# Kernel tuning notes

Hardware: AMD Instinct MI355X
Metric: run time of the kernel (lower is better)

The kernel has to match this reference:

```python
import jax, jax.numpy as jnp
import numpy as np
from jax import lax

T = 1.0      # terminal time
SIGMA = 1.0  # diffusion coefficient
N, D, P, M, H = 16384, 16, 8, 50, 128


def setup_inputs() -> dict:
    key = jax.random.key(0)
    ks = jax.random.split(key, 8)
    scale1 = 1.0 / np.sqrt(1 + D + P)
    scale2 = 1.0 / np.sqrt(H)
    return {
        "initial_states": jax.random.normal(ks[0], (N, D), jnp.float32),
        "initial_values": jax.random.normal(ks[1], (N,), jnp.float32),
        "observations": jax.random.normal(ks[2], (N, P), jnp.float32),
        "noise": jax.random.normal(ks[3], (M, N, D), jnp.float32),
        "W1": jax.random.normal(ks[4], (1 + D + P, H), jnp.float32) * scale1,
        "b1": jnp.zeros((H,), jnp.float32),
        "W2": jax.random.normal(ks[5], (H, H), jnp.float32) * scale2,
        "b2": jnp.zeros((H,), jnp.float32),
        "W3": jax.random.normal(ks[6], (H, D), jnp.float32) * scale2,
        "b3": jnp.zeros((D,), jnp.float32),
    }


def reference(initial_states, initial_values, observations, noise,
              W1, b1, W2, b2, W3, b3):
    """Euler-Maruyama rollout of simulate_SDEs: joint (X, V) SDE with
    per-step Z-network drift. drift b(X) = -X (OU process)."""
    m_steps = noise.shape[0]
    dt = jnp.asarray(T / m_steps, initial_states.dtype)
    sqrt_dt = jnp.sqrt(dt)
    times = jnp.arange(m_steps, dtype=initial_states.dtype) * dt  # time[m]

    def z_net(t, X, Y):
        tcol = jnp.full((X.shape[0], 1), t, X.dtype)
        h = jnp.concatenate([tcol, X, Y], axis=1)      # (N, 1+d+p)
        h = jax.nn.relu(h @ W1 + b1)
        h = jax.nn.relu(h @ W2 + b2)
        return h @ W3 + b3                             # (N, d)

    def step(carry, inp):
        X, V = carry
        eps, t = inp
        Wn = sqrt_dt * eps                             # Brownian increment
        Z = z_net(t, X, observations)
        drift_V = 0.5 * jnp.sum(Z * Z, axis=1)
        V = V + dt * drift_V + jnp.sum(Z * Wn, axis=1)
        X = X + dt * (-X) + SIGMA * Wn                 # b(X) = -X
        return (X, V), None

    (X, V), _ = lax.scan(step, (initial_states, initial_values), (noise, times))
    return X, V
```

## Files before the change

### kernel.cpp

```cpp
#include <hip/hip_runtime.h>

typedef __bf16   bf16x8 __attribute__((ext_vector_type(8)));
typedef float    f32x4  __attribute__((ext_vector_type(4)));
typedef float    f32x2  __attribute__((ext_vector_type(2)));
typedef uint32_t u32x4  __attribute__((ext_vector_type(4)));

constexpr int N_ = 16384;
constexpr int D_ = 16;
constexpr int P_ = 8;
constexpr int H_ = 128;
constexpr int M_ = 50;

__device__ __forceinline__ uint32_t pk_bf16(float a, float b) {
    uint32_t ua = __builtin_bit_cast(uint32_t, a) + 0x8000u;
    uint32_t ub = __builtin_bit_cast(uint32_t, b) + 0x8000u;
    return __builtin_amdgcn_perm(ub, ua, 0x07060302u);
}
__device__ __forceinline__ uint32_t cvtpk(float a, float b) {
    uint32_t r;
    asm("v_cvt_pk_bf16_f32 %0, %1, %2" : "=v"(r) : "v"(a), "v"(b));
    return r;
}
__device__ __forceinline__ uint32_t cvtpk_relu(float a, float b) {
    return cvtpk(fmaxf(a, 0.0f), fmaxf(b, 0.0f));
}

__global__ __launch_bounds__(64, 1)
void sde_fused(const float* __restrict__ X0,
               const float* __restrict__ V0,
               const float* __restrict__ Yobs,
               const float* __restrict__ noise,
               const float* __restrict__ W1, const float* __restrict__ b1,
               const float* __restrict__ W2, const float* __restrict__ b2,
               const float* __restrict__ W3, const float* __restrict__ b3,
               float* __restrict__ out)
{
    const int lane = threadIdx.x;
    const int n    = lane & 15;
    const int q    = lane >> 4;
    const int gr   = blockIdx.x * 16 + n;

    const float dt   = 0.02f;
    const float sqdt = 0.1414213562373095f;

    bf16x8 w1f[8];
#pragma unroll
    for (int ct = 0; ct < 8; ++ct) {
        u32x4 u;
        u[0] = pk_bf16(W1[(1 + q * 4 + 0) * H_ + ct * 16 + n],
                       W1[(1 + q * 4 + 1) * H_ + ct * 16 + n]);
        u[1] = pk_bf16(W1[(1 + q * 4 + 2) * H_ + ct * 16 + n],
                       W1[(1 + q * 4 + 3) * H_ + ct * 16 + n]);
        u[2] = pk_bf16(W1[(17 + q * 2 + 0) * H_ + ct * 16 + n],
                       W1[(17 + q * 2 + 1) * H_ + ct * 16 + n]);
        u[3] = (q == 0) ? pk_bf16(b1[ct * 16 + n], W1[ct * 16 + n]) : 0u;
        w1f[ct] = __builtin_bit_cast(bf16x8, u);
    }
    bf16x8 w2f[8][4];
#pragma unroll
    for (int ct = 0; ct < 8; ++ct)
#pragma unroll
        for (int kt = 0; kt < 4; ++kt) {
            u32x4 u;
#pragma unroll
            for (int w = 0; w < 4; ++w) {
                int h0 = (kt * 2 + (w >> 1)) * 16 + q * 4 + (w & 1) * 2;
                u[w] = pk_bf16(W2[h0 * H_ + ct * 16 + n],
                               W2[(h0 + 1) * H_ + ct * 16 + n]);
            }
            w2f[ct][kt] = __builtin_bit_cast(bf16x8, u);
        }
    bf16x8 w3f[4];
#pragma unroll
    for (int kt = 0; kt < 4; ++kt) {
        u32x4 u;
#pragma unroll
        for (int w = 0; w < 4; ++w) {
            int h0 = (kt * 2 + (w >> 1)) * 16 + q * 4 + (w & 1) * 2;
            u[w] = pk_bf16(W3[h0 * D_ + n], W3[(h0 + 1) * D_ + n]);
        }
        w3f[kt] = __builtin_bit_cast(bf16x8, u);
    }
    f32x4 b2r[8];
#pragma unroll
    for (int ct = 0; ct < 8; ++ct)
#pragma unroll
        for (int r = 0; r < 4; ++r) b2r[ct][r] = b2[ct * 16 + q * 4 + r];
    f32x4 b3r;
#pragma unroll
    for (int r = 0; r < 4; ++r) b3r[r] = b3[q * 4 + r];

    f32x4 x = *(const f32x4*)&X0[gr * D_ + q * 4];
    f32x2 y2 = *(const f32x2*)&Yobs[gr * P_ + q * 2];
    const uint32_t yw = pk_bf16(y2[0], y2[1]);

    const float* npb = noise + (size_t)gr * D_ + q * 4;
    f32x4 e0 = *(const f32x4*)npb;
    f32x4 e1 = *(const f32x4*)(npb + (size_t)N_ * D_);
    float vaccA = 0.0f, vaccB = 0.0f;

#pragma unroll 1
    for (int mm = 0; mm < M_; mm += 2) {
        const int p0 = (mm + 2 < M_) ? (mm + 2) : (M_ - 1);
        const int p1 = (mm + 3 < M_) ? (mm + 3) : (M_ - 1);
        f32x4 eN0 = *(const f32x4*)(npb + (size_t)p0 * N_ * D_);
        f32x4 eN1 = *(const f32x4*)(npb + (size_t)p1 * N_ * D_);

        const float tA = (float)mm * dt;
        const float tB = (float)(mm + 1) * dt;

        f32x4 xB;
#pragma unroll
        for (int r = 0; r < 4; ++r) xB[r] = fmaf(x[r], 0.98f, sqdt * e0[r]);

        u32x4 auA;
        auA[0] = cvtpk(x[0], x[1]);
        auA[1] = cvtpk(x[2], x[3]);
        auA[2] = yw;
        auA[3] = (q == 0) ? cvtpk(1.0f, tA) : 0u;
        bf16x8 a0A = __builtin_bit_cast(bf16x8, auA);
        u32x4 auB;
        auB[0] = cvtpk(xB[0], xB[1]);
        auB[1] = cvtpk(xB[2], xB[3]);
        auB[2] = yw;
        auB[3] = (q == 0) ? cvtpk(1.0f, tB) : 0u;
        bf16x8 a0B = __builtin_bit_cast(bf16x8, auB);

        f32x4 h1cA[8], h1cB[8];
#pragma unroll
        for (int ct = 0; ct < 8; ++ct)
            h1cA[ct] = __builtin_amdgcn_mfma_f32_16x16x32_bf16(
                w1f[ct], a0A, (f32x4){0.f, 0.f, 0.f, 0.f}, 0, 0, 0);
#pragma unroll
        for (int ct = 0; ct < 8; ++ct)
            h1cB[ct] = __builtin_amdgcn_mfma_f32_16x16x32_bf16(
                w1f[ct], a0B, (f32x4){0.f, 0.f, 0.f, 0.f}, 0, 0, 0);

        bf16x8 h1bA[4], h1bB[4];
#pragma unroll
        for (int kt = 0; kt < 4; ++kt) {
            u32x4 u;
            u[0] = cvtpk_relu(h1cA[2 * kt][0], h1cA[2 * kt][1]);
            u[1] = cvtpk_relu(h1cA[2 * kt][2], h1cA[2 * kt][3]);
            u[2] = cvtpk_relu(h1cA[2 * kt + 1][0], h1cA[2 * kt + 1][1]);
            u[3] = cvtpk_relu(h1cA[2 * kt + 1][2], h1cA[2 * kt + 1][3]);
            h1bA[kt] = __builtin_bit_cast(bf16x8, u);
        }
#pragma unroll
        for (int kt = 0; kt < 4; ++kt) {
            u32x4 u;
            u[0] = cvtpk_relu(h1cB[2 * kt][0], h1cB[2 * kt][1]);
            u[1] = cvtpk_relu(h1cB[2 * kt][2], h1cB[2 * kt][3]);
            u[2] = cvtpk_relu(h1cB[2 * kt + 1][0], h1cB[2 * kt + 1][1]);
            u[3] = cvtpk_relu(h1cB[2 * kt + 1][2], h1cB[2 * kt + 1][3]);
            h1bB[kt] = __builtin_bit_cast(bf16x8, u);
        }

        f32x4 h2cA[8], h2cB[8];
#pragma unroll
        for (int ct = 0; ct < 8; ++ct) {
            f32x4 c = b2r[ct];
#pragma unroll
            for (int kt = 0; kt < 4; ++kt)
                c = __builtin_amdgcn_mfma_f32_16x16x32_bf16(
                    w2f[ct][kt], h1bA[kt], c, 0, 0, 0);
            h2cA[ct] = c;
        }
#pragma unroll
        for (int ct = 0; ct < 8; ++ct) {
            f32x4 c = b2r[ct];
#pragma unroll
            for (int kt = 0; kt < 4; ++kt)
                c = __builtin_amdgcn_mfma_f32_16x16x32_bf16(
                    w2f[ct][kt], h1bB[kt], c, 0, 0, 0);
            h2cB[ct] = c;
        }

        bf16x8 h2bA[4], h2bB[4];
#pragma unroll
        for (int kt = 0; kt < 4; ++kt) {
            u32x4 u;
            u[0] = cvtpk_relu(h2cA[2 * kt][0], h2cA[2 * kt][1]);
            u[1] = cvtpk_relu(h2cA[2 * kt][2], h2cA[2 * kt][3]);
            u[2] = cvtpk_relu(h2cA[2 * kt + 1][0], h2cA[2 * kt + 1][1]);
            u[3] = cvtpk_relu(h2cA[2 * kt + 1][2], h2cA[2 * kt + 1][3]);
            h2bA[kt] = __builtin_bit_cast(bf16x8, u);
        }
#pragma unroll
        for (int kt = 0; kt < 4; ++kt) {
            u32x4 u;
            u[0] = cvtpk_relu(h2cB[2 * kt][0], h2cB[2 * kt][1]);
            u[1] = cvtpk_relu(h2cB[2 * kt][2], h2cB[2 * kt][3]);
            u[2] = cvtpk_relu(h2cB[2 * kt + 1][0], h2cB[2 * kt + 1][1]);
            u[3] = cvtpk_relu(h2cB[2 * kt + 1][2], h2cB[2 * kt + 1][3]);
            h2bB[kt] = __builtin_bit_cast(bf16x8, u);
        }

        f32x4 zaA = __builtin_amdgcn_mfma_f32_16x16x32_bf16(w3f[0], h2bA[0], b3r, 0, 0, 0);
        zaA = __builtin_amdgcn_mfma_f32_16x16x32_bf16(w3f[1], h2bA[1], zaA, 0, 0, 0);
        f32x4 zbA = __builtin_amdgcn_mfma_f32_16x16x32_bf16(
            w3f[2], h2bA[2], (f32x4){0.f, 0.f, 0.f, 0.f}, 0, 0, 0);
        zbA = __builtin_amdgcn_mfma_f32_16x16x32_bf16(w3f[3], h2bA[3], zbA, 0, 0, 0);
        f32x4 zaB = __builtin_amdgcn_mfma_f32_16x16x32_bf16(w3f[0], h2bB[0], b3r, 0, 0, 0);
        zaB = __builtin_amdgcn_mfma_f32_16x16x32_bf16(w3f[1], h2bB[1], zaB, 0, 0, 0);
        f32x4 zbB = __builtin_amdgcn_mfma_f32_16x16x32_bf16(
            w3f[2], h2bB[2], (f32x4){0.f, 0.f, 0.f, 0.f}, 0, 0, 0);
        zbB = __builtin_amdgcn_mfma_f32_16x16x32_bf16(w3f[3], h2bB[3], zbB, 0, 0, 0);

#pragma unroll
        for (int r = 0; r < 4; ++r) {
            float zA  = zaA[r] + zbA[r];
            float wnA = sqdt * e0[r];
            vaccA = fmaf(zA, wnA, fmaf(0.01f * zA, zA, vaccA));
            float zB  = zaB[r] + zbB[r];
            float wnB = sqdt * e1[r];
            vaccB = fmaf(zB, wnB, fmaf(0.01f * zB, zB, vaccB));
            x[r] = fmaf(xB[r], 0.98f, wnB);
        }

        e0 = eN0; e1 = eN1;
    }

    float part = vaccA + vaccB;
    part += __shfl_xor(part, 16);
    part += __shfl_xor(part, 32);
    float v = V0[gr] + part;

    *(f32x4*)&out[gr * D_ + q * 4] = x;
    if (q == 0) out[N_ * D_ + gr] = v;
}

extern "C" void kernel_launch(void* const* d_in, const int* in_sizes, int n_in,
                              void* d_out, int out_size, void* d_ws, size_t ws_size,
                              hipStream_t stream)
{
    const float* X0 = (const float*)d_in[0];
    const float* V0 = (const float*)d_in[1];
    const float* Y  = (const float*)d_in[2];
    const float* nz = (const float*)d_in[3];
    const float* W1 = (const float*)d_in[4];
    const float* b1 = (const float*)d_in[5];
    const float* W2 = (const float*)d_in[6];
    const float* b2 = (const float*)d_in[7];
    const float* W3 = (const float*)d_in[8];
    const float* b3 = (const float*)d_in[9];
    float* out = (float*)d_out;

    sde_fused<<<N_ / 16, 64, 0, stream>>>(X0, V0, Y, nz, W1, b1, W2, b2, W3, b3, out);
}
```

Measured before the change: 156.6 us.

## Split time loop across two waves and move W2 weights to LDS

Each block now runs two waves. The second wave fast-forwards X through the first 26 steps (X does not depend on Z), so the two waves evaluate the MLP over disjoint halves of the time steps, and V partials are combined through shared memory. W2 fragments and b2 are staged in LDS and streamed with double buffering instead of held in registers. This frees registers for two blocks per CU and shortens the serial chain, at the cost of LDS traffic and a redundant X pre-roll.

Result: faster. 152.0 us (-2.9%).

```diff
diff --git a/kernel.cpp b/kernel.cpp
--- a/kernel.cpp
+++ b/kernel.cpp
@@ -25,7 +25,16 @@
     return cvtpk(fmaxf(a, 0.0f), fmaxf(b, 0.0f));
 }
 
-__global__ __launch_bounds__(64, 1)
+__device__ __forceinline__ bf16x8 lds_ldv8(const void* p) {
+    u32x4 v = *(volatile const u32x4*)p;
+    return __builtin_bit_cast(bf16x8, v);
+}
+__device__ __forceinline__ f32x4 lds_ldvf(const void* p) {
+    u32x4 v = *(volatile const u32x4*)p;
+    return __builtin_bit_cast(f32x4, v);
+}
+
+__global__ __launch_bounds__(128, 2)
 void sde_fused(const float* __restrict__ X0,
                const float* __restrict__ V0,
                const float* __restrict__ Yobs,
@@ -35,13 +44,37 @@
                const float* __restrict__ W3, const float* __restrict__ b3,
                float* __restrict__ out)
 {
-    const int lane = threadIdx.x;
+    const int tid  = threadIdx.x;
+    const int lane = tid & 63;
+    const int half = tid >> 6;
     const int n    = lane & 15;
     const int q    = lane >> 4;
     const int gr   = blockIdx.x * 16 + n;
 
     const float dt   = 0.02f;
     const float sqdt = 0.1414213562373095f;
+
+    __shared__ bf16x8 w2lds[8][4][64];
+    __shared__ float  b2lds[H_];
+    __shared__ float  vpart[16];
+
+#pragma unroll
+    for (int cc = 0; cc < 4; ++cc) {
+        const int ct = half * 4 + cc;
+#pragma unroll
+        for (int kt = 0; kt < 4; ++kt) {
+            u32x4 u;
+#pragma unroll
+            for (int w = 0; w < 4; ++w) {
+                int h0 = (kt * 2 + (w >> 1)) * 16 + q * 4 + (w & 1) * 2;
+                u[w] = pk_bf16(W2[h0 * H_ + ct * 16 + n],
+                               W2[(h0 + 1) * H_ + ct * 16 + n]);
+            }
+            w2lds[ct][kt][lane] = __builtin_bit_cast(bf16x8, u);
+        }
+    }
+    if (half == 0 && lane < 32)
+        *(f32x4*)&b2lds[lane * 4] = *(const f32x4*)&b2[lane * 4];
 
     bf16x8 w1f[8];
 #pragma unroll
@@ -56,20 +89,6 @@
         u[3] = (q == 0) ? pk_bf16(b1[ct * 16 + n], W1[ct * 16 + n]) : 0u;
         w1f[ct] = __builtin_bit_cast(bf16x8, u);
     }
-    bf16x8 w2f[8][4];
-#pragma unroll
-    for (int ct = 0; ct < 8; ++ct)
-#pragma unroll
-        for (int kt = 0; kt < 4; ++kt) {
-            u32x4 u;
-#pragma unroll
-            for (int w = 0; w < 4; ++w) {
-                int h0 = (kt * 2 + (w >> 1)) * 16 + q * 4 + (w & 1) * 2;
-                u[w] = pk_bf16(W2[h0 * H_ + ct * 16 + n],
-                               W2[(h0 + 1) * H_ + ct * 16 + n]);
-            }
-            w2f[ct][kt] = __builtin_bit_cast(bf16x8, u);
-        }
     bf16x8 w3f[4];
 #pragma unroll
     for (int kt = 0; kt < 4; ++kt) {
@@ -81,37 +100,52 @@
         }
         w3f[kt] = __builtin_bit_cast(bf16x8, u);
     }
-    f32x4 b2r[8];
-#pragma unroll
-    for (int ct = 0; ct < 8; ++ct)
-#pragma unroll
-        for (int r = 0; r < 4; ++r) b2r[ct][r] = b2[ct * 16 + q * 4 + r];
-    f32x4 b3r;
-#pragma unroll
-    for (int r = 0; r < 4; ++r) b3r[r] = b3[q * 4 + r];
+    f32x4 b3r = *(const f32x4*)&b3[q * 4];
+
+    __syncthreads();
 
     f32x4 x = *(const f32x4*)&X0[gr * D_ + q * 4];
     f32x2 y2 = *(const f32x2*)&Yobs[gr * P_ + q * 2];
     const uint32_t yw = pk_bf16(y2[0], y2[1]);
-
     const float* npb = noise + (size_t)gr * D_ + q * 4;
-    f32x4 e0 = *(const f32x4*)npb;
-    f32x4 e1 = *(const f32x4*)(npb + (size_t)N_ * D_);
+
+    if (half == 1) {
+#pragma unroll 2
+        for (int m = 0; m < 26; ++m) {
+            f32x4 e = *(const f32x4*)(npb + (size_t)m * N_ * D_);
+#pragma unroll
+            for (int r = 0; r < 4; ++r)
+                x[r] = fmaf(x[r], 0.98f, sqdt * e[r]);
+        }
+    }
+
+    const int start  = half ? 26 : 0;
+    const int npairs = half ? 12 : 13;
+
+    f32x4 e0 = *(const f32x4*)(npb + (size_t)start * N_ * D_);
+    f32x4 e1 = *(const f32x4*)(npb + (size_t)(start + 1) * N_ * D_);
     float vaccA = 0.0f, vaccB = 0.0f;
 
 #pragma unroll 1
-    for (int mm = 0; mm < M_; mm += 2) {
-        const int p0 = (mm + 2 < M_) ? (mm + 2) : (M_ - 1);
-        const int p1 = (mm + 3 < M_) ? (mm + 3) : (M_ - 1);
-        f32x4 eN0 = *(const f32x4*)(npb + (size_t)p0 * N_ * D_);
-        f32x4 eN1 = *(const f32x4*)(npb + (size_t)p1 * N_ * D_);
-
-        const float tA = (float)mm * dt;
-        const float tB = (float)(mm + 1) * dt;
+    for (int p = 0; p < npairs; ++p) {
+        const int mA = start + 2 * p;
+        const int p2 = (mA + 2 < M_) ? (mA + 2) : (M_ - 1);
+        const int p3 = (mA + 3 < M_) ? (mA + 3) : (M_ - 1);
+        f32x4 e2 = *(const f32x4*)(npb + (size_t)p2 * N_ * D_);
+        f32x4 e3 = *(const f32x4*)(npb + (size_t)p3 * N_ * D_);
+
+        const float tA = (float)mA * dt;
+        const float tB = (float)(mA + 1) * dt;
 
         f32x4 xB;
 #pragma unroll
         for (int r = 0; r < 4; ++r) xB[r] = fmaf(x[r], 0.98f, sqdt * e0[r]);
+
+        bf16x8 wb[2][4];
+#pragma unroll
+        for (int kt = 0; kt < 4; ++kt) wb[0][kt] = lds_ldv8(&w2lds[0][kt][lane]);
+        f32x4 cb[2];
+        cb[0] = lds_ldvf(&b2lds[q * 4]);
 
         u32x4 auA;
         auA[0] = cvtpk(x[0], x[1]);
@@ -126,17 +160,12 @@
         auB[3] = (q == 0) ? cvtpk(1.0f, tB) : 0u;
         bf16x8 a0B = __builtin_bit_cast(bf16x8, auB);
 
-        f32x4 h1cA[8], h1cB[8];
+        f32x4 h1cA[8];
 #pragma unroll
         for (int ct = 0; ct < 8; ++ct)
             h1cA[ct] = __builtin_amdgcn_mfma_f32_16x16x32_bf16(
                 w1f[ct], a0A, (f32x4){0.f, 0.f, 0.f, 0.f}, 0, 0, 0);
-#pragma unroll
-        for (int ct = 0; ct < 8; ++ct)
-            h1cB[ct] = __builtin_amdgcn_mfma_f32_16x16x32_bf16(
-                w1f[ct], a0B, (f32x4){0.f, 0.f, 0.f, 0.f}, 0, 0, 0);
-
-        bf16x8 h1bA[4], h1bB[4];
+        bf16x8 h1bA[4];
 #pragma unroll
         for (int kt = 0; kt < 4; ++kt) {
             u32x4 u;
@@ -146,6 +175,12 @@
             u[3] = cvtpk_relu(h1cA[2 * kt + 1][2], h1cA[2 * kt + 1][3]);
             h1bA[kt] = __builtin_bit_cast(bf16x8, u);
         }
+        f32x4 h1cB[8];
+#pragma unroll
+        for (int ct = 0; ct < 8; ++ct)
+            h1cB[ct] = __builtin_amdgcn_mfma_f32_16x16x32_bf16(
+                w1f[ct], a0B, (f32x4){0.f, 0.f, 0.f, 0.f}, 0, 0, 0);
+        bf16x8 h1bB[4];
 #pragma unroll
         for (int kt = 0; kt < 4; ++kt) {
             u32x4 u;
@@ -156,44 +191,42 @@
             h1bB[kt] = __builtin_bit_cast(bf16x8, u);
         }
 
-        f32x4 h2cA[8], h2cB[8];
+        bf16x8 h2bA[4], h2bB[4];
+        f32x4 hpA, hpB;
 #pragma unroll
         for (int ct = 0; ct < 8; ++ct) {
-            f32x4 c = b2r[ct];
+            if (ct < 7) {
+#pragma unroll
+                for (int kt = 0; kt < 4; ++kt)
+                    wb[(ct + 1) & 1][kt] = lds_ldv8(&w2lds[ct + 1][kt][lane]);
+                cb[(ct + 1) & 1] = lds_ldvf(&b2lds[(ct + 1) * 16 + q * 4]);
+            }
+            f32x4 cA = cb[ct & 1];
+            f32x4 cB = cA;
 #pragma unroll
             for (int kt = 0; kt < 4; ++kt)
-                c = __builtin_amdgcn_mfma_f32_16x16x32_bf16(
-                    w2f[ct][kt], h1bA[kt], c, 0, 0, 0);
-            h2cA[ct] = c;
-        }
-#pragma unroll
-        for (int ct = 0; ct < 8; ++ct) {
-            f32x4 c = b2r[ct];
+                cA = __builtin_amdgcn_mfma_f32_16x16x32_bf16(
+                    wb[ct & 1][kt], h1bA[kt], cA, 0, 0, 0);
 #pragma unroll
             for (int kt = 0; kt < 4; ++kt)
-                c = __builtin_amdgcn_mfma_f32_16x16x32_bf16(
-                    w2f[ct][kt], h1bB[kt], c, 0, 0, 0);
-            h2cB[ct] = c;
-        }
-
-        bf16x8 h2bA[4], h2bB[4];
-#pragma unroll
-        for (int kt = 0; kt < 4; ++kt) {
-            u32x4 u;
-            u[0] = cvtpk_relu(h2cA[2 * kt][0], h2cA[2 * kt][1]);
-            u[1] = cvtpk_relu(h2cA[2 * kt][2], h2cA[2 * kt][3]);
-            u[2] = cvtpk_relu(h2cA[2 * kt + 1][0], h2cA[2 * kt + 1][1]);
-            u[3] = cvtpk_relu(h2cA[2 * kt + 1][2], h2cA[2 * kt + 1][3]);
-            h2bA[kt] = __builtin_bit_cast(bf16x8, u);
-        }
-#pragma unroll
-        for (int kt = 0; kt < 4; ++kt) {
-            u32x4 u;
-            u[0] = cvtpk_relu(h2cB[2 * kt][0], h2cB[2 * kt][1]);
-            u[1] = cvtpk_relu(h2cB[2 * kt][2], h2cB[2 * kt][3]);
-            u[2] = cvtpk_relu(h2cB[2 * kt + 1][0], h2cB[2 * kt + 1][1]);
-            u[3] = cvtpk_relu(h2cB[2 * kt + 1][2], h2cB[2 * kt + 1][3]);
-            h2bB[kt] = __builtin_bit_cast(bf16x8, u);
+                cB = __builtin_amdgcn_mfma_f32_16x16x32_bf16(
+                    wb[ct & 1][kt], h1bB[kt], cB, 0, 0, 0);
+            if ((ct & 1) == 0) {
+                hpA = cA; hpB = cB;
+            } else {
+                u32x4 uA;
+                uA[0] = cvtpk_relu(hpA[0], hpA[1]);
+                uA[1] = cvtpk_relu(hpA[2], hpA[3]);
+                uA[2] = cvtpk_relu(cA[0], cA[1]);
+                uA[3] = cvtpk_relu(cA[2], cA[3]);
+                h2bA[ct >> 1] = __builtin_bit_cast(bf16x8, uA);
+                u32x4 uB;
+                uB[0] = cvtpk_relu(hpB[0], hpB[1]);
+                uB[1] = cvtpk_relu(hpB[2], hpB[3]);
+                uB[2] = cvtpk_relu(cB[0], cB[1]);
+                uB[3] = cvtpk_relu(cB[2], cB[3]);
+                h2bB[ct >> 1] = __builtin_bit_cast(bf16x8, uB);
+            }
         }
 
         f32x4 zaA = __builtin_amdgcn_mfma_f32_16x16x32_bf16(w3f[0], h2bA[0], b3r, 0, 0, 0);
@@ -218,16 +251,19 @@
             x[r] = fmaf(xB[r], 0.98f, wnB);
         }
 
-        e0 = eN0; e1 = eN1;
+        e0 = e2; e1 = e3;
     }
 
     float part = vaccA + vaccB;
     part += __shfl_xor(part, 16);
     part += __shfl_xor(part, 32);
-    float v = V0[gr] + part;
-
-    *(f32x4*)&out[gr * D_ + q * 4] = x;
-    if (q == 0) out[N_ * D_ + gr] = v;
+
+    if (half == 0 && q == 0) vpart[n] = part;
+    __syncthreads();
+    if (half == 1) {
+        *(f32x4*)&out[gr * D_ + q * 4] = x;
+        if (q == 0) out[N_ * D_ + gr] = V0[gr] + vpart[n] + part;
+    }
 }
 
 extern "C" void kernel_launch(void* const* d_in, const int* in_sizes, int n_in,
@@ -246,5 +282,5 @@
     const float* b3 = (const float*)d_in[9];
     float* out = (float*)d_out;
 
-    sde_fused<<<N_ / 16, 64, 0, stream>>>(X0, V0, Y, nz, W1, b1, W2, b2, W3, b3, out);
-}
+    sde_fused<<<N_ / 16, 128, 0, stream>>>(X0, V0, Y, nz, W1, b1, W2, b2, W3, b3, out);
+}
```
